# Kernel tuning notes

Hardware: AMD Instinct MI355X
Metric: run time of the kernel (lower is better)

## Reference

```python
import jax, jax.numpy as jnp
import numpy as np

B, L, H, D = 8, 4800, 8, 64  # L = 60*80 tokens, D = head_dim = self.dim


def setup_inputs() -> dict:
    key = jax.random.key(0)
    ks = jax.random.split(key, 8)
    q = jax.random.normal(ks[0], (B, L, H, D), jnp.float32)
    k = jax.random.normal(ks[1], (B, L, H, D), jnp.float32)
    v = jax.random.normal(ks[2], (B, L, H, D), jnp.float32)
    temperature = jnp.ones((H, 1, 1), jnp.float32)          # nn.Parameter(torch.ones(H,1,1))
    attns = jnp.ones((4,), jnp.float32)                      # four scalar gate params (init 1.0)
    # Conv1d(dim,1,k=1): weight [1, dim, 1] -> store as [dim]; bias [1]
    row_w = 0.1 * jax.random.normal(ks[3], (D,), jnp.float32)
    row_b = 0.1 * jax.random.normal(ks[4], (1,), jnp.float32)
    col_w = 0.1 * jax.random.normal(ks[5], (D,), jnp.float32)
    col_b = 0.1 * jax.random.normal(ks[6], (1,), jnp.float32)
    return {"q": q, "k": k, "v": v, "temperature": temperature, "attns": attns,
            "row_w": row_w, "row_b": row_b, "col_w": col_w, "col_b": col_b}


def _l2norm(x):
    # torch F.normalize(dim=-1): x / max(||x||, eps)
    n = jnp.sqrt(jnp.sum(x * x, axis=-1, keepdims=True))
    return x / jnp.maximum(n, 1e-12)


def reference(q, k, v, temperature, attns, row_w, row_b, col_w, col_b):
    # [B,L,H,D] -> [B,H,D,L]
    qt = _l2norm(q.transpose(0, 2, 3, 1))
    kt = _l2norm(k.transpose(0, 2, 3, 1))
    vt = v.transpose(0, 2, 3, 1)
    # channel attention: [B,H,D,D]
    attn = jnp.einsum('bhdl,bhel->bhde', qt, kt)
    # col_conv: Conv1d over C1 rows -> gate per column; row_conv: over C2 -> gate per row
    w_col = jax.nn.sigmoid(jnp.einsum('bhce,c->bhe', attn, col_w) + col_b)[:, :, None, :]  # [B,H,1,C]
    w_row = jax.nn.sigmoid(jnp.einsum('bhce,e->bhc', attn, row_w) + row_b)[:, :, :, None]  # [B,H,C,1]
    attn = (attn * w_col + attn * w_row) * temperature[None]  # temperature [H,1,1] broadcasts
    C = attn.shape[-1]
    neg_inf = jnp.array(-jnp.inf, attn.dtype)
    out = jnp.zeros_like(vt)  # [B,H,D,L]
    for i, tk in enumerate([C // 2, (2 * C) // 3, (3 * C) // 4, (4 * C) // 5]):
        thr = jax.lax.top_k(attn, tk)[0][..., -1:]           # kth largest per row
        a = jnp.where(attn >= thr, attn, neg_inf)            # keep top-k entries
        a = jax.nn.softmax(a, axis=-1)
        out = out + attns[i] * jnp.einsum('bhde,bhel->bhdl', a, vt)
    # rearrange 'b head c (h w) -> b (head c) h w' then back to [B, L, head, c]
    return out.transpose(0, 3, 1, 2)  # [B,L,H,D]
```

## Files before the change

### kernel.cpp

```cpp
#include <hip/hip_runtime.h>

#define B_ 8
#define L_ 4800
#define H_ 8
#define D_ 64
#define BH_ 64

#define G_ELEMS (BH_*D_*D_)
#define QSQ_OFF G_ELEMS
#define KSQ_OFF (QSQ_OFF + BH_*D_)
#define M_OFF   (KSQ_OFF + BH_*D_)

#define NCH 12
#define CHUNK (L_/NCH)

__global__ __launch_bounds__(256) void gram_kernel(
    const float* __restrict__ q, const float* __restrict__ k,
    float* __restrict__ G, float* __restrict__ qsq, float* __restrict__ ksq)
{
  const int bh = blockIdx.y;
  const int b = bh >> 3, h = bh & 7;
  const int l0 = blockIdx.x * CHUNK;
  const int t = threadIdx.x;
  const int tx = t & 15, ty = t >> 4;

  __shared__ float Lq[8][64];
  __shared__ float Lk[8][64];

  const int sr = (t & 127) >> 4;
  const int sc = (t & 15) * 4;
  const bool isQ = (t < 128);
  const float* __restrict__ src = isQ ? q : k;
  const float* sp = src + (((size_t)(b*L_ + l0 + sr))*H_ + h)*D_ + sc;

  float sq0=0.f, sq1=0.f, sq2=0.f, sq3=0.f;
  float acc[4][4] = {};

  for (int ls = 0; ls < CHUNK; ls += 8) {
    float4 v4 = *(const float4*)sp;
    sp += 8*H_*D_;
    __syncthreads();
    *(float4*)(isQ ? &Lq[sr][sc] : &Lk[sr][sc]) = v4;
    sq0 += v4.x*v4.x; sq1 += v4.y*v4.y; sq2 += v4.z*v4.z; sq3 += v4.w*v4.w;
    __syncthreads();
#pragma unroll
    for (int r = 0; r < 8; r++) {
      float4 qa4 = *(const float4*)&Lq[r][ty*4];
      float4 kb4 = *(const float4*)&Lk[r][tx*4];
      float qa[4] = {qa4.x,qa4.y,qa4.z,qa4.w};
      float kb[4] = {kb4.x,kb4.y,kb4.z,kb4.w};
#pragma unroll
      for (int i = 0; i < 4; i++)
#pragma unroll
        for (int j = 0; j < 4; j++)
          acc[i][j] = fmaf(qa[i], kb[j], acc[i][j]);
    }
  }

  float* nacc = isQ ? qsq : ksq;
  atomicAdd(&nacc[bh*64 + sc + 0], sq0);
  atomicAdd(&nacc[bh*64 + sc + 1], sq1);
  atomicAdd(&nacc[bh*64 + sc + 2], sq2);
  atomicAdd(&nacc[bh*64 + sc + 3], sq3);

  float* g = G + (size_t)bh*4096;
#pragma unroll
  for (int i = 0; i < 4; i++)
#pragma unroll
    for (int j = 0; j < 4; j++)
      atomicAdd(&g[(ty*4+i)*64 + tx*4 + j], acc[i][j]);
}

__global__ __launch_bounds__(256) void mask_kernel(
    const float* __restrict__ G, const float* __restrict__ qsq,
    const float* __restrict__ ksq,
    const float* __restrict__ temperature, const float* __restrict__ attns,
    const float* __restrict__ row_w, const float* __restrict__ row_b,
    const float* __restrict__ col_w, const float* __restrict__ col_b,
    float* __restrict__ M)
{
  const int bh = blockIdx.x;
  const int h = bh & 7;
  const int t = threadIdx.x;
  const int d = t & 63, q4 = t >> 6;
  const int e0 = q4 * 16;

  __shared__ float att[64][65];
  __shared__ float rnq[64], rnk[64], cw[64], rw[64];
  __shared__ float wcol[64], wrow[64];
  __shared__ float thr[4][64];
  __shared__ float pmax[4][64];
  __shared__ float rowmax[64];
  __shared__ float psum[4][4][64];
  __shared__ float rinv[4][64];

  if (t < 64)        rnq[t]     = 1.0f / fmaxf(sqrtf(qsq[bh*64 + t]), 1e-12f);
  else if (t < 128)  rnk[t-64]  = 1.0f / fmaxf(sqrtf(ksq[bh*64 + t-64]), 1e-12f);
  else if (t < 192)  cw[t-128]  = col_w[t-128];
  else               rw[t-192]  = row_w[t-192];
  __syncthreads();

  {
    const float* gp = G + (size_t)bh*4096 + d*64 + e0;
    float rq = rnq[d];
#pragma unroll
    for (int ee = 0; ee < 16; ee++)
      att[d][e0+ee] = gp[ee] * rq * rnk[e0+ee];
  }
  __syncthreads();

  if (t < 64) {
    float s = 0.f;
    for (int c = 0; c < 64; c++) s += att[c][t] * cw[c];
    s += col_b[0];
    wcol[t] = 1.0f / (1.0f + __expf(-s));
  } else if (t < 128) {
    int c = t - 64;
    float s = 0.f;
    for (int e = 0; e < 64; e++) s += att[c][e] * rw[e];
    s += row_b[0];
    wrow[c] = 1.0f / (1.0f + __expf(-s));
  }
  __syncthreads();

  {
    const float temp = temperature[h];
    const float wr = wrow[d];
    float mx = -1e30f;
#pragma unroll
    for (int ee = 0; ee < 16; ee++) {
      float x = att[d][e0+ee] * ((wcol[e0+ee] + wr) * temp);
      att[d][e0+ee] = x;
      mx = fmaxf(mx, x);
    }
    pmax[q4][d] = mx;
  }
  __syncthreads();
  if (t < 64)
    rowmax[t] = fmaxf(fmaxf(pmax[0][t], pmax[1][t]), fmaxf(pmax[2][t], pmax[3][t]));

  {
    float x[16];
#pragma unroll
    for (int j = 0; j < 16; j++) x[j] = att[d][e0+j];
    int gt[16] = {}, ge[16] = {};
    for (int m = 0; m < 64; m++) {
      float y = att[d][m];
#pragma unroll
      for (int j = 0; j < 16; j++) { gt[j] += (y > x[j]); ge[j] += (y >= x[j]); }
    }
    const int tks[4] = {32, 42, 48, 51};
#pragma unroll
    for (int j = 0; j < 16; j++)
#pragma unroll
      for (int i = 0; i < 4; i++)
        if (gt[j] <= tks[i]-1 && ge[j] >= tks[i]) thr[i][d] = x[j];
  }
  __syncthreads();

  {
    const float rm = rowmax[d];
    const float t0 = thr[0][d], t1 = thr[1][d], t2 = thr[2][d], t3 = thr[3][d];
    float s0=0.f, s1=0.f, s2=0.f, s3=0.f;
#pragma unroll
    for (int ee = 0; ee < 16; ee++) {
      float xv = att[d][e0+ee];
      float ex = __expf(xv - rm);
      if (xv >= t0) s0 += ex;
      if (xv >= t1) s1 += ex;
      if (xv >= t2) s2 += ex;
      if (xv >= t3) s3 += ex;
    }
    psum[q4][0][d] = s0; psum[q4][1][d] = s1; psum[q4][2][d] = s2; psum[q4][3][d] = s3;
  }
  __syncthreads();
  if (t < 64) {
#pragma unroll
    for (int i = 0; i < 4; i++) {
      float s = psum[0][i][t] + psum[1][i][t] + psum[2][i][t] + psum[3][i][t];
      rinv[i][t] = attns[i] / s;
    }
  }
  __syncthreads();

  {
    const float rm = rowmax[d];
    const float t0 = thr[0][d], t1 = thr[1][d], t2 = thr[2][d], t3 = thr[3][d];
    const float r0 = rinv[0][d], r1 = rinv[1][d], r2 = rinv[2][d], r3 = rinv[3][d];
    float* mo = M + (size_t)bh*4096 + d*64 + e0;
#pragma unroll
    for (int ee = 0; ee < 16; ee++) {
      float xv = att[d][e0+ee];
      float ex = __expf(xv - rm);
      float m = 0.f;
      if (xv >= t0) m += r0 * ex;
      if (xv >= t1) m += r1 * ex;
      if (xv >= t2) m += r2 * ex;
      if (xv >= t3) m += r3 * ex;
      mo[ee] = m;
    }
  }
}

__global__ __launch_bounds__(256) void apply_kernel(
    const float* __restrict__ M, const float* __restrict__ v,
    float* __restrict__ out)
{
  const int bh = blockIdx.y;
  const int b = bh >> 3, h = bh & 7;
  const int l0 = blockIdx.x * 64;
  const int t = threadIdx.x;

  __shared__ float Ms[64][68];
  __shared__ float Vs[64][68];

#pragma unroll
  for (int i = 0; i < 4; i++) {
    int idx = t + i*256;
    int dd = idx >> 4;
    int c4 = (idx & 15) * 4;
    float4 mv = *(const float4*)(M + (size_t)bh*4096 + dd*64 + c4);
    Ms[c4+0][dd] = mv.x; Ms[c4+1][dd] = mv.y; Ms[c4+2][dd] = mv.z; Ms[c4+3][dd] = mv.w;
    float4 vv = *(const float4*)(v + (((size_t)b*L_ + l0 + dd)*H_ + h)*D_ + c4);
    *(float4*)&Vs[dd][c4] = vv;
  }
  __syncthreads();

  const int dq = t & 15, lq = t >> 4;
  const int d0 = dq * 4, lr = lq * 4;
  float acc[4][4] = {};

#pragma unroll
  for (int e4 = 0; e4 < 16; e4++) {
    const int e = e4 * 4;
    float4 m0 = *(const float4*)&Ms[e+0][d0];
    float4 m1 = *(const float4*)&Ms[e+1][d0];
    float4 m2 = *(const float4*)&Ms[e+2][d0];
    float4 m3 = *(const float4*)&Ms[e+3][d0];
    float ma[4][4] = {{m0.x,m0.y,m0.z,m0.w},{m1.x,m1.y,m1.z,m1.w},
                      {m2.x,m2.y,m2.z,m2.w},{m3.x,m3.y,m3.z,m3.w}};
#pragma unroll
    for (int j = 0; j < 4; j++) {
      float4 vj = *(const float4*)&Vs[lr+j][e];
      float va[4] = {vj.x, vj.y, vj.z, vj.w};
#pragma unroll
      for (int i = 0; i < 4; i++) {
        acc[i][j] = fmaf(ma[0][i], va[0], acc[i][j]);
        acc[i][j] = fmaf(ma[1][i], va[1], acc[i][j]);
        acc[i][j] = fmaf(ma[2][i], va[2], acc[i][j]);
        acc[i][j] = fmaf(ma[3][i], va[3], acc[i][j]);
      }
    }
  }

#pragma unroll
  for (int j = 0; j < 4; j++) {
    int l = l0 + lr + j;
    float4 o = make_float4(acc[0][j], acc[1][j], acc[2][j], acc[3][j]);
    *(float4*)(out + (((size_t)b*L_ + l)*H_ + h)*D_ + d0) = o;
  }
}

extern "C" void kernel_launch(void* const* d_in, const int* in_sizes, int n_in,
                              void* d_out, int out_size, void* d_ws, size_t ws_size,
                              hipStream_t stream) {
  const float* q           = (const float*)d_in[0];
  const float* k           = (const float*)d_in[1];
  const float* v           = (const float*)d_in[2];
  const float* temperature = (const float*)d_in[3];
  const float* attns       = (const float*)d_in[4];
  const float* row_w       = (const float*)d_in[5];
  const float* row_b       = (const float*)d_in[6];
  const float* col_w       = (const float*)d_in[7];
  const float* col_b       = (const float*)d_in[8];
  float* out = (float*)d_out;

  float* ws  = (float*)d_ws;
  float* G   = ws;
  float* qsq = ws + QSQ_OFF;
  float* ksq = ws + KSQ_OFF;
  float* M   = ws + M_OFF;

  hipMemsetAsync(ws, 0, (size_t)M_OFF * sizeof(float), stream);

  gram_kernel<<<dim3(NCH, BH_), 256, 0, stream>>>(q, k, G, qsq, ksq);
  mask_kernel<<<dim3(BH_), 256, 0, stream>>>(G, qsq, ksq, temperature, attns,
                                             row_w, row_b, col_w, col_b, M);
  apply_kernel<<<dim3(L_/64, BH_), 256, 0, stream>>>(M, v, out);
}
```

Before: 357.2 us.

## Double-buffer gram and apply kernels with register prefetch and fewer atomics

The gram kernel now has every thread load both q and k in 16-row slabs, with double-buffered shared memory and register prefetch. Grid chunks grow to 25 per head, and the per-column square-norm atomics are reduced through shared memory before they are issued. The apply kernel now processes three 64-token tiles per block and reuses the M transpose across them, prefetching the next V tile into registers while computing the current one. This is meant to hide global load latency and cut the number of sync and atomic operations, at the cost of fewer blocks and more shared memory and registers.

```diff
diff --git a/kernel.cpp b/kernel.cpp
--- a/kernel.cpp
+++ b/kernel.cpp
@@ -11,8 +11,9 @@
 #define KSQ_OFF (QSQ_OFF + BH_*D_)
 #define M_OFF   (KSQ_OFF + BH_*D_)
 
-#define NCH 12
-#define CHUNK (L_/NCH)
+#define NCH 25
+#define CHUNK 192
+#define NSLAB 12
 
 __global__ __launch_bounds__(256) void gram_kernel(
     const float* __restrict__ q, const float* __restrict__ k,
@@ -24,29 +25,36 @@
   const int t = threadIdx.x;
   const int tx = t & 15, ty = t >> 4;
 
-  __shared__ float Lq[8][64];
-  __shared__ float Lk[8][64];
-
-  const int sr = (t & 127) >> 4;
+  __shared__ float Lq[2][16][64];
+  __shared__ float Lk[2][16][64];
+
+  const int sr = t >> 4;
   const int sc = (t & 15) * 4;
-  const bool isQ = (t < 128);
-  const float* __restrict__ src = isQ ? q : k;
-  const float* sp = src + (((size_t)(b*L_ + l0 + sr))*H_ + h)*D_ + sc;
-
-  float sq0=0.f, sq1=0.f, sq2=0.f, sq3=0.f;
+  const float* qp = q + (((size_t)(b*L_ + l0 + sr))*H_ + h)*D_ + sc;
+  const float* kp = k + (((size_t)(b*L_ + l0 + sr))*H_ + h)*D_ + sc;
+  const size_t step = (size_t)16*H_*D_;
+
+  float sq[4] = {0,0,0,0}, sk[4] = {0,0,0,0};
   float acc[4][4] = {};
 
-  for (int ls = 0; ls < CHUNK; ls += 8) {
-    float4 v4 = *(const float4*)sp;
-    sp += 8*H_*D_;
-    __syncthreads();
-    *(float4*)(isQ ? &Lq[sr][sc] : &Lk[sr][sc]) = v4;
-    sq0 += v4.x*v4.x; sq1 += v4.y*v4.y; sq2 += v4.z*v4.z; sq3 += v4.w*v4.w;
-    __syncthreads();
-#pragma unroll
-    for (int r = 0; r < 8; r++) {
-      float4 qa4 = *(const float4*)&Lq[r][ty*4];
-      float4 kb4 = *(const float4*)&Lk[r][tx*4];
+  float4 rq = *(const float4*)qp; qp += step;
+  float4 rk = *(const float4*)kp; kp += step;
+  *(float4*)&Lq[0][sr][sc] = rq;
+  *(float4*)&Lk[0][sr][sc] = rk;
+  sq[0] += rq.x*rq.x; sq[1] += rq.y*rq.y; sq[2] += rq.z*rq.z; sq[3] += rq.w*rq.w;
+  sk[0] += rk.x*rk.x; sk[1] += rk.y*rk.y; sk[2] += rk.z*rk.z; sk[3] += rk.w*rk.w;
+  __syncthreads();
+
+  for (int s = 0; s < NSLAB; s++) {
+    const int cur = s & 1;
+    if (s + 1 < NSLAB) {
+      rq = *(const float4*)qp; qp += step;
+      rk = *(const float4*)kp; kp += step;
+    }
+#pragma unroll
+    for (int r = 0; r < 16; r++) {
+      float4 qa4 = *(const float4*)&Lq[cur][r][ty*4];
+      float4 kb4 = *(const float4*)&Lk[cur][r][tx*4];
       float qa[4] = {qa4.x,qa4.y,qa4.z,qa4.w};
       float kb[4] = {kb4.x,kb4.y,kb4.z,kb4.w};
 #pragma unroll
@@ -55,13 +63,30 @@
         for (int j = 0; j < 4; j++)
           acc[i][j] = fmaf(qa[i], kb[j], acc[i][j]);
     }
-  }
-
-  float* nacc = isQ ? qsq : ksq;
-  atomicAdd(&nacc[bh*64 + sc + 0], sq0);
-  atomicAdd(&nacc[bh*64 + sc + 1], sq1);
-  atomicAdd(&nacc[bh*64 + sc + 2], sq2);
-  atomicAdd(&nacc[bh*64 + sc + 3], sq3);
+    if (s + 1 < NSLAB) {
+      *(float4*)&Lq[cur^1][sr][sc] = rq;
+      *(float4*)&Lk[cur^1][sr][sc] = rk;
+      sq[0] += rq.x*rq.x; sq[1] += rq.y*rq.y; sq[2] += rq.z*rq.z; sq[3] += rq.w*rq.w;
+      sk[0] += rk.x*rk.x; sk[1] += rk.y*rk.y; sk[2] += rk.z*rk.z; sk[3] += rk.w*rk.w;
+      __syncthreads();
+    }
+  }
+
+  *(float4*)&Lq[0][sr][sc] = make_float4(sq[0], sq[1], sq[2], sq[3]);
+  *(float4*)&Lk[0][sr][sc] = make_float4(sk[0], sk[1], sk[2], sk[3]);
+  __syncthreads();
+  if (t < 64) {
+    float s = 0.f;
+#pragma unroll
+    for (int r = 0; r < 16; r++) s += Lq[0][r][t];
+    atomicAdd(&qsq[bh*64 + t], s);
+  } else if (t < 128) {
+    const int d = t - 64;
+    float s = 0.f;
+#pragma unroll
+    for (int r = 0; r < 16; r++) s += Lk[0][r][d];
+    atomicAdd(&ksq[bh*64 + d], s);
+  }
 
   float* g = G + (size_t)bh*4096;
 #pragma unroll
@@ -202,62 +227,89 @@
   }
 }
 
+#define ATILES 3
+#define ABLK 25
+
 __global__ __launch_bounds__(256) void apply_kernel(
     const float* __restrict__ M, const float* __restrict__ v,
     float* __restrict__ out)
 {
   const int bh = blockIdx.y;
   const int b = bh >> 3, h = bh & 7;
-  const int l0 = blockIdx.x * 64;
+  const int lbase = blockIdx.x * (64 * ATILES);
   const int t = threadIdx.x;
 
   __shared__ float Ms[64][68];
-  __shared__ float Vs[64][68];
+  __shared__ float Vs[2][64][68];
+
+  const int dd = t >> 4;
+  const int c4 = (t & 15) * 4;
 
 #pragma unroll
   for (int i = 0; i < 4; i++) {
-    int idx = t + i*256;
-    int dd = idx >> 4;
-    int c4 = (idx & 15) * 4;
-    float4 mv = *(const float4*)(M + (size_t)bh*4096 + dd*64 + c4);
-    Ms[c4+0][dd] = mv.x; Ms[c4+1][dd] = mv.y; Ms[c4+2][dd] = mv.z; Ms[c4+3][dd] = mv.w;
-    float4 vv = *(const float4*)(v + (((size_t)b*L_ + l0 + dd)*H_ + h)*D_ + c4);
-    *(float4*)&Vs[dd][c4] = vv;
-  }
+    int row = dd + i*16;
+    float4 mv = *(const float4*)(M + (size_t)bh*4096 + row*64 + c4);
+    Ms[c4+0][row] = mv.x; Ms[c4+1][row] = mv.y;
+    Ms[c4+2][row] = mv.z; Ms[c4+3][row] = mv.w;
+  }
+
+  float4 pv[4];
+#pragma unroll
+  for (int i = 0; i < 4; i++)
+    pv[i] = *(const float4*)(v + (((size_t)b*L_ + lbase + dd + i*16)*H_ + h)*D_ + c4);
+#pragma unroll
+  for (int i = 0; i < 4; i++)
+    *(float4*)&Vs[0][dd + i*16][c4] = pv[i];
   __syncthreads();
 
   const int dq = t & 15, lq = t >> 4;
   const int d0 = dq * 4, lr = lq * 4;
-  float acc[4][4] = {};
-
-#pragma unroll
-  for (int e4 = 0; e4 < 16; e4++) {
-    const int e = e4 * 4;
-    float4 m0 = *(const float4*)&Ms[e+0][d0];
-    float4 m1 = *(const float4*)&Ms[e+1][d0];
-    float4 m2 = *(const float4*)&Ms[e+2][d0];
-    float4 m3 = *(const float4*)&Ms[e+3][d0];
-    float ma[4][4] = {{m0.x,m0.y,m0.z,m0.w},{m1.x,m1.y,m1.z,m1.w},
-                      {m2.x,m2.y,m2.z,m2.w},{m3.x,m3.y,m3.z,m3.w}};
+
+  for (int s = 0; s < ATILES; s++) {
+    const int cur = s & 1;
+    if (s + 1 < ATILES) {
+#pragma unroll
+      for (int i = 0; i < 4; i++)
+        pv[i] = *(const float4*)(v + (((size_t)b*L_ + lbase + (s+1)*64 + dd + i*16)*H_ + h)*D_ + c4);
+    }
+
+    float acc[4][4] = {};
+#pragma unroll
+    for (int e4 = 0; e4 < 16; e4++) {
+      const int e = e4 * 4;
+      float4 m0 = *(const float4*)&Ms[e+0][d0];
+      float4 m1 = *(const float4*)&Ms[e+1][d0];
+      float4 m2 = *(const float4*)&Ms[e+2][d0];
+      float4 m3 = *(const float4*)&Ms[e+3][d0];
+      float ma[4][4] = {{m0.x,m0.y,m0.z,m0.w},{m1.x,m1.y,m1.z,m1.w},
+                        {m2.x,m2.y,m2.z,m2.w},{m3.x,m3.y,m3.z,m3.w}};
+#pragma unroll
+      for (int j = 0; j < 4; j++) {
+        float4 vj = *(const float4*)&Vs[cur][lr+j][e];
+        float va[4] = {vj.x, vj.y, vj.z, vj.w};
+#pragma unroll
+        for (int i = 0; i < 4; i++) {
+          acc[i][j] = fmaf(ma[0][i], va[0], acc[i][j]);
+          acc[i][j] = fmaf(ma[1][i], va[1], acc[i][j]);
+          acc[i][j] = fmaf(ma[2][i], va[2], acc[i][j]);
+          acc[i][j] = fmaf(ma[3][i], va[3], acc[i][j]);
+        }
+      }
+    }
+
 #pragma unroll
     for (int j = 0; j < 4; j++) {
-      float4 vj = *(const float4*)&Vs[lr+j][e];
-      float va[4] = {vj.x, vj.y, vj.z, vj.w};
-#pragma unroll
-      for (int i = 0; i < 4; i++) {
-        acc[i][j] = fmaf(ma[0][i], va[0], acc[i][j]);
-        acc[i][j] = fmaf(ma[1][i], va[1], acc[i][j]);
-        acc[i][j] = fmaf(ma[2][i], va[2], acc[i][j]);
-        acc[i][j] = fmaf(ma[3][i], va[3], acc[i][j]);
-      }
-    }
-  }
-
-#pragma unroll
-  for (int j = 0; j < 4; j++) {
-    int l = l0 + lr + j;
-    float4 o = make_float4(acc[0][j], acc[1][j], acc[2][j], acc[3][j]);
-    *(float4*)(out + (((size_t)b*L_ + l)*H_ + h)*D_ + d0) = o;
+      int l = lbase + s*64 + lr + j;
+      float4 o = make_float4(acc[0][j], acc[1][j], acc[2][j], acc[3][j]);
+      *(float4*)(out + (((size_t)b*L_ + l)*H_ + h)*D_ + d0) = o;
+    }
+
+    if (s + 1 < ATILES) {
+#pragma unroll
+      for (int i = 0; i < 4; i++)
+        *(float4*)&Vs[cur^1][dd + i*16][c4] = pv[i];
+      __syncthreads();
+    }
   }
 }
 
@@ -286,5 +338,5 @@
   gram_kernel<<<dim3(NCH, BH_), 256, 0, stream>>>(q, k, G, qsq, ksq);
   mask_kernel<<<dim3(BH_), 256, 0, stream>>>(G, qsq, ksq, temperature, attns,
                                              row_w, row_b, col_w, col_b, M);
-  apply_kernel<<<dim3(L_/64, BH_), 256, 0, stream>>>(M, v, out);
+  apply_kernel<<<dim3(ABLK, BH_), 256, 0, stream>>>(M, v, out);
 }
```

Result: slower. 385.8 us (+8.0%).

## Restructure gram kernel with per-wave 64x64 tiles, double buffering, partial-sum outputs

Applied to the files above, without the earlier changes.

The gram kernel now gives each wave a full 64x64 accumulator, with an 8x8 register tile per lane, over its own slabs of L. Slabs are double-buffered in shared memory with a register prefetch, so there are no block-wide barriers inside the main loop. Per-chunk partial Gram matrices and squared norms are written to workspace instead of being combined with global atomics, which removes the memset. The mask kernel sums the 15 partials. This costs much higher register pressure (64 accumulators per lane) and more workspace traffic.

```diff
diff --git a/kernel.cpp b/kernel.cpp
--- a/kernel.cpp
+++ b/kernel.cpp
@@ -6,74 +6,159 @@
 #define D_ 64
 #define BH_ 64
 
-#define G_ELEMS (BH_*D_*D_)
-#define QSQ_OFF G_ELEMS
-#define KSQ_OFF (QSQ_OFF + BH_*D_)
-#define M_OFF   (KSQ_OFF + BH_*D_)
-
-#define NCH 12
-#define CHUNK (L_/NCH)
+#define NCH 15
+#define CHUNK 320
+#define SLAB 8
+#define WSLABS 10
+
+#define GP_SIZE   (BH_*NCH*4096)
+#define QSQP_OFF  GP_SIZE
+#define QSQP_SIZE (BH_*NCH*64)
+#define KSQP_OFF  (QSQP_OFF + QSQP_SIZE)
+#define M_OFF     (KSQP_OFF + QSQP_SIZE)
 
 __global__ __launch_bounds__(256) void gram_kernel(
     const float* __restrict__ q, const float* __restrict__ k,
-    float* __restrict__ G, float* __restrict__ qsq, float* __restrict__ ksq)
+    float* __restrict__ Gp, float* __restrict__ qsqp, float* __restrict__ ksqp)
 {
   const int bh = blockIdx.y;
   const int b = bh >> 3, h = bh & 7;
-  const int l0 = blockIdx.x * CHUNK;
+  const int cx = blockIdx.x;
+  const int l0 = cx * CHUNK;
   const int t = threadIdx.x;
-  const int tx = t & 15, ty = t >> 4;
-
-  __shared__ float Lq[8][64];
-  __shared__ float Lk[8][64];
-
-  const int sr = (t & 127) >> 4;
-  const int sc = (t & 15) * 4;
-  const bool isQ = (t < 128);
-  const float* __restrict__ src = isQ ? q : k;
-  const float* sp = src + (((size_t)(b*L_ + l0 + sr))*H_ + h)*D_ + sc;
-
-  float sq0=0.f, sq1=0.f, sq2=0.f, sq3=0.f;
-  float acc[4][4] = {};
-
-  for (int ls = 0; ls < CHUNK; ls += 8) {
-    float4 v4 = *(const float4*)sp;
-    sp += 8*H_*D_;
-    __syncthreads();
-    *(float4*)(isQ ? &Lq[sr][sc] : &Lk[sr][sc]) = v4;
-    sq0 += v4.x*v4.x; sq1 += v4.y*v4.y; sq2 += v4.z*v4.z; sq3 += v4.w*v4.w;
-    __syncthreads();
-#pragma unroll
-    for (int r = 0; r < 8; r++) {
-      float4 qa4 = *(const float4*)&Lq[r][ty*4];
-      float4 kb4 = *(const float4*)&Lk[r][tx*4];
-      float qa[4] = {qa4.x,qa4.y,qa4.z,qa4.w};
-      float kb[4] = {kb4.x,kb4.y,kb4.z,kb4.w};
-#pragma unroll
-      for (int i = 0; i < 4; i++)
-#pragma unroll
-        for (int j = 0; j < 4; j++)
-          acc[i][j] = fmaf(qa[i], kb[j], acc[i][j]);
-    }
-  }
-
-  float* nacc = isQ ? qsq : ksq;
-  atomicAdd(&nacc[bh*64 + sc + 0], sq0);
-  atomicAdd(&nacc[bh*64 + sc + 1], sq1);
-  atomicAdd(&nacc[bh*64 + sc + 2], sq2);
-  atomicAdd(&nacc[bh*64 + sc + 3], sq3);
-
-  float* g = G + (size_t)bh*4096;
-#pragma unroll
-  for (int i = 0; i < 4; i++)
-#pragma unroll
-    for (int j = 0; j < 4; j++)
-      atomicAdd(&g[(ty*4+i)*64 + tx*4 + j], acc[i][j]);
+  const int w = t >> 6, lane = t & 63;
+
+  __shared__ float Ls[4][2][2][SLAB][64];
+
+  const int lrow = lane >> 4;
+  const int lcol = (lane & 15) * 4;
+  const int r0 = (lane >> 3) * 8;
+  const int c0 = (lane & 7) * 8;
+
+  const float* qb = q + (size_t)(b*L_)*512 + h*64;
+  const float* kb = k + (size_t)(b*L_)*512 + h*64;
+
+  float accG[8][8] = {};
+  float sqq[4] = {0,0,0,0}, sqk[4] = {0,0,0,0};
+
+  {
+    const int ls = l0 + w*SLAB;
+    const float* qp = qb + (size_t)(ls + lrow)*512 + lcol;
+    const float* kp = kb + (size_t)(ls + lrow)*512 + lcol;
+    float4 a0 = *(const float4*)qp;
+    float4 a1 = *(const float4*)(qp + 4*512);
+    float4 b0 = *(const float4*)kp;
+    float4 b1 = *(const float4*)(kp + 4*512);
+    sqq[0]+=a0.x*a0.x; sqq[1]+=a0.y*a0.y; sqq[2]+=a0.z*a0.z; sqq[3]+=a0.w*a0.w;
+    sqq[0]+=a1.x*a1.x; sqq[1]+=a1.y*a1.y; sqq[2]+=a1.z*a1.z; sqq[3]+=a1.w*a1.w;
+    sqk[0]+=b0.x*b0.x; sqk[1]+=b0.y*b0.y; sqk[2]+=b0.z*b0.z; sqk[3]+=b0.w*b0.w;
+    sqk[0]+=b1.x*b1.x; sqk[1]+=b1.y*b1.y; sqk[2]+=b1.z*b1.z; sqk[3]+=b1.w*b1.w;
+    *(float4*)&Ls[w][0][0][lrow  ][lcol] = a0;
+    *(float4*)&Ls[w][0][0][lrow+4][lcol] = a1;
+    *(float4*)&Ls[w][0][1][lrow  ][lcol] = b0;
+    *(float4*)&Ls[w][0][1][lrow+4][lcol] = b1;
+  }
+
+  for (int s = 0; s < WSLABS; s++) {
+    const int cur = s & 1;
+    float4 a0, a1, b0, b1;
+    if (s + 1 < WSLABS) {
+      const int ls = l0 + (w + 4*(s+1))*SLAB;
+      const float* qp = qb + (size_t)(ls + lrow)*512 + lcol;
+      const float* kp = kb + (size_t)(ls + lrow)*512 + lcol;
+      a0 = *(const float4*)qp;
+      a1 = *(const float4*)(qp + 4*512);
+      b0 = *(const float4*)kp;
+      b1 = *(const float4*)(kp + 4*512);
+    }
+    const float (*Lq)[64] = Ls[w][cur][0];
+    const float (*Lk)[64] = Ls[w][cur][1];
+#pragma unroll
+    for (int r = 0; r < SLAB; r++) {
+      float4 qa0 = *(const float4*)&Lq[r][r0];
+      float4 qa1 = *(const float4*)&Lq[r][r0+4];
+      float4 kb0 = *(const float4*)&Lk[r][c0];
+      float4 kb1 = *(const float4*)&Lk[r][c0+4];
+      float av[8] = {qa0.x,qa0.y,qa0.z,qa0.w,qa1.x,qa1.y,qa1.z,qa1.w};
+      float bv[8] = {kb0.x,kb0.y,kb0.z,kb0.w,kb1.x,kb1.y,kb1.z,kb1.w};
+#pragma unroll
+      for (int i = 0; i < 8; i++)
+#pragma unroll
+        for (int j = 0; j < 8; j++)
+          accG[i][j] = fmaf(av[i], bv[j], accG[i][j]);
+    }
+    if (s + 1 < WSLABS) {
+      sqq[0]+=a0.x*a0.x; sqq[1]+=a0.y*a0.y; sqq[2]+=a0.z*a0.z; sqq[3]+=a0.w*a0.w;
+      sqq[0]+=a1.x*a1.x; sqq[1]+=a1.y*a1.y; sqq[2]+=a1.z*a1.z; sqq[3]+=a1.w*a1.w;
+      sqk[0]+=b0.x*b0.x; sqk[1]+=b0.y*b0.y; sqk[2]+=b0.z*b0.z; sqk[3]+=b0.w*b0.w;
+      sqk[0]+=b1.x*b1.x; sqk[1]+=b1.y*b1.y; sqk[2]+=b1.z*b1.z; sqk[3]+=b1.w*b1.w;
+      *(float4*)&Ls[w][cur^1][0][lrow  ][lcol] = a0;
+      *(float4*)&Ls[w][cur^1][0][lrow+4][lcol] = a1;
+      *(float4*)&Ls[w][cur^1][1][lrow  ][lcol] = b0;
+      *(float4*)&Ls[w][cur^1][1][lrow+4][lcol] = b1;
+    }
+  }
+
+  float* red = &Ls[0][0][0][0][0];
+  float4* redf4 = (float4*)red;
+  float* gout = Gp + ((size_t)bh*NCH + cx)*4096;
+
+  __syncthreads();
+  if (r0 < 32) {
+#pragma unroll
+    for (int i = 0; i < 8; i++) {
+      *(float4*)&red[w*2048 + (r0+i)*64 + c0    ] = make_float4(accG[i][0],accG[i][1],accG[i][2],accG[i][3]);
+      *(float4*)&red[w*2048 + (r0+i)*64 + c0 + 4] = make_float4(accG[i][4],accG[i][5],accG[i][6],accG[i][7]);
+    }
+  }
+  __syncthreads();
+#pragma unroll
+  for (int pp = 0; pp < 2; pp++) {
+    int fi = t + pp*256;
+    float4 s0 = redf4[fi], s1 = redf4[512+fi], s2 = redf4[1024+fi], s3 = redf4[1536+fi];
+    float4 r; r.x = s0.x+s1.x+s2.x+s3.x; r.y = s0.y+s1.y+s2.y+s3.y;
+    r.z = s0.z+s1.z+s2.z+s3.z; r.w = s0.w+s1.w+s2.w+s3.w;
+    *(float4*)&gout[fi*4] = r;
+  }
+  __syncthreads();
+  if (r0 >= 32) {
+#pragma unroll
+    for (int i = 0; i < 8; i++) {
+      *(float4*)&red[w*2048 + (r0-32+i)*64 + c0    ] = make_float4(accG[i][0],accG[i][1],accG[i][2],accG[i][3]);
+      *(float4*)&red[w*2048 + (r0-32+i)*64 + c0 + 4] = make_float4(accG[i][4],accG[i][5],accG[i][6],accG[i][7]);
+    }
+  }
+  __syncthreads();
+#pragma unroll
+  for (int pp = 0; pp < 2; pp++) {
+    int fi = t + pp*256;
+    float4 s0 = redf4[fi], s1 = redf4[512+fi], s2 = redf4[1024+fi], s3 = redf4[1536+fi];
+    float4 r; r.x = s0.x+s1.x+s2.x+s3.x; r.y = s0.y+s1.y+s2.y+s3.y;
+    r.z = s0.z+s1.z+s2.z+s3.z; r.w = s0.w+s1.w+s2.w+s3.w;
+    *(float4*)&gout[2048 + fi*4] = r;
+  }
+  __syncthreads();
+  redf4[w*64 + lane]       = make_float4(sqq[0],sqq[1],sqq[2],sqq[3]);
+  redf4[256 + w*64 + lane] = make_float4(sqk[0],sqk[1],sqk[2],sqk[3]);
+  __syncthreads();
+  if (t < 128) {
+    const int d = t & 63;
+    const int col4 = d >> 2, c = d & 3;
+    const int base = (t < 64) ? 0 : 1024;
+    float s = 0.f;
+#pragma unroll
+    for (int ww = 0; ww < 4; ww++)
+#pragma unroll
+      for (int m = 0; m < 4; m++)
+        s += red[base + (ww*64 + m*16 + col4)*4 + c];
+    float* dst = (t < 64) ? qsqp : ksqp;
+    dst[((size_t)bh*NCH + cx)*64 + d] = s;
+  }
 }
 
 __global__ __launch_bounds__(256) void mask_kernel(
-    const float* __restrict__ G, const float* __restrict__ qsq,
-    const float* __restrict__ ksq,
+    const float* __restrict__ Gp, const float* __restrict__ qsqp,
+    const float* __restrict__ ksqp,
     const float* __restrict__ temperature, const float* __restrict__ attns,
     const float* __restrict__ row_w, const float* __restrict__ row_b,
     const float* __restrict__ col_w, const float* __restrict__ col_b,
@@ -94,18 +179,35 @@
   __shared__ float psum[4][4][64];
   __shared__ float rinv[4][64];
 
-  if (t < 64)        rnq[t]     = 1.0f / fmaxf(sqrtf(qsq[bh*64 + t]), 1e-12f);
-  else if (t < 128)  rnk[t-64]  = 1.0f / fmaxf(sqrtf(ksq[bh*64 + t-64]), 1e-12f);
-  else if (t < 192)  cw[t-128]  = col_w[t-128];
-  else               rw[t-192]  = row_w[t-192];
-  __syncthreads();
-
-  {
-    const float* gp = G + (size_t)bh*4096 + d*64 + e0;
-    float rq = rnq[d];
-#pragma unroll
-    for (int ee = 0; ee < 16; ee++)
-      att[d][e0+ee] = gp[ee] * rq * rnk[e0+ee];
+  if (t < 64) {
+    float s = 0.f;
+    for (int c = 0; c < NCH; c++) s += qsqp[((size_t)bh*NCH + c)*64 + t];
+    rnq[t] = 1.0f / fmaxf(sqrtf(s), 1e-12f);
+  } else if (t < 128) {
+    float s = 0.f;
+    for (int c = 0; c < NCH; c++) s += ksqp[((size_t)bh*NCH + c)*64 + (t-64)];
+    rnk[t-64] = 1.0f / fmaxf(sqrtf(s), 1e-12f);
+  } else if (t < 192) {
+    cw[t-128] = col_w[t-128];
+  } else {
+    rw[t-192] = row_w[t-192];
+  }
+  __syncthreads();
+
+  {
+    const float rq = rnq[d];
+#pragma unroll
+    for (int ee = 0; ee < 16; ee += 4) {
+      float4 g = make_float4(0.f,0.f,0.f,0.f);
+      for (int c = 0; c < NCH; c++) {
+        float4 gc = *(const float4*)&Gp[((size_t)bh*NCH + c)*4096 + d*64 + e0 + ee];
+        g.x += gc.x; g.y += gc.y; g.z += gc.z; g.w += gc.w;
+      }
+      att[d][e0+ee+0] = g.x * rq * rnk[e0+ee+0];
+      att[d][e0+ee+1] = g.y * rq * rnk[e0+ee+1];
+      att[d][e0+ee+2] = g.z * rq * rnk[e0+ee+2];
+      att[d][e0+ee+3] = g.w * rq * rnk[e0+ee+3];
+    }
   }
   __syncthreads();
 
@@ -275,16 +377,15 @@
   const float* col_b       = (const float*)d_in[8];
   float* out = (float*)d_out;
 
-  float* ws  = (float*)d_ws;
-  float* G   = ws;
-  float* qsq = ws + QSQ_OFF;
-  float* ksq = ws + KSQ_OFF;
-  float* M   = ws + M_OFF;
-
-  hipMemsetAsync(ws, 0, (size_t)M_OFF * sizeof(float), stream);
-
-  gram_kernel<<<dim3(NCH, BH_), 256, 0, stream>>>(q, k, G, qsq, ksq);
-  mask_kernel<<<dim3(BH_), 256, 0, stream>>>(G, qsq, ksq, temperature, attns,
+  float* ws   = (float*)d_ws;
+  float* Gp   = ws;
+  float* qsqp = ws + QSQP_OFF;
+  float* ksqp = ws + KSQP_OFF;
+  float* M    = ws + M_OFF;
+
+
+  gram_kernel<<<dim3(NCH, BH_), 256, 0, stream>>>(q, k, Gp, qsqp, ksqp);
+  mask_kernel<<<dim3(BH_), 256, 0, stream>>>(Gp, qsqp, ksqp, temperature, attns,
                                              row_w, row_b, col_w, col_b, M);
   apply_kernel<<<dim3(L_/64, BH_), 256, 0, stream>>>(M, v, out);
 }
```

Measured after the change: 305.8 us. 1.17x faster.
